# Performance work log

Hardware: AMD Instinct MI355X
Metric: run time of the kernel (lower is better)

Reference implementation:

```python
import jax, jax.numpy as jnp
import numpy as np

CHANNELS = 512
GROUPS = 32
EPS = 1e-5


def setup_inputs() -> dict:
    key = jax.random.key(0)
    ks = jax.random.split(key, 7)
    C = CHANNELS
    x = jax.random.normal(ks[0], (32, C, 32, 32), dtype=jnp.float32)
    norm_w = jax.random.normal(ks[1], (C,), dtype=jnp.float32) * 0.02 + 1.0
    norm_b = jax.random.normal(ks[2], (C,), dtype=jnp.float32) * 0.02
    # 1x1 convs stored as (out_channels, in_channels)
    qkv_w = jax.random.normal(ks[3], (3 * C, C), dtype=jnp.float32) * (C ** -0.5)
    qkv_b = jax.random.normal(ks[4], (3 * C,), dtype=jnp.float32) * 0.02
    proj_w = jax.random.normal(ks[5], (C, C), dtype=jnp.float32) * (C ** -0.5)
    proj_b = jax.random.normal(ks[6], (C,), dtype=jnp.float32) * 0.02
    return {"x": x, "norm_w": norm_w, "norm_b": norm_b,
            "qkv_w": qkv_w, "qkv_b": qkv_b,
            "proj_w": proj_w, "proj_b": proj_b}


def _group_norm(x, w, b):
    B, C, H, W = x.shape
    xg = x.reshape(B, GROUPS, C // GROUPS, H, W)
    mean = xg.mean(axis=(2, 3, 4), keepdims=True)
    var = xg.var(axis=(2, 3, 4), keepdims=True)
    xn = ((xg - mean) * jax.lax.rsqrt(var + EPS)).reshape(B, C, H, W)
    return xn * w[None, :, None, None] + b[None, :, None, None]


def reference(x, norm_w, norm_b, qkv_w, qkv_b, proj_w, proj_b):
    B, C, H, W = x.shape
    scale = C ** (-0.5)
    h = _group_norm(x, norm_w, norm_b)
    # 1x1 conv == per-pixel linear: (B,C,H,W) -> (B,3C,H,W)
    qkv = jnp.einsum('bchw,oc->bohw', h, qkv_w) + qkv_b[None, :, None, None]
    qkv = qkv.reshape(B, 3, C, H * W)
    q, k, v = qkv[:, 0], qkv[:, 1], qkv[:, 2]  # each (B, C, N)
    # attn[b, i, j] = softmax_j( q[:, i] . k[:, j] * scale )
    scores = jnp.einsum('bcn,bcm->bnm', q, k) * scale  # (B, N, N)
    attn = jax.nn.softmax(scores, axis=-1)
    # h[b, c, i] = sum_j v[b, c, j] * attn[b, i, j]
    hout = jnp.einsum('bcm,bnm->bcn', v, attn).reshape(B, C, H, W)
    out = x + jnp.einsum('bchw,oc->bohw', hout, proj_w) + proj_b[None, :, None, None]
    return out
```

## Files before the change

kernel.cpp:

```cpp
#include <hip/hip_runtime.h>
#include <math.h>

#define B_ 32
#define C_ 512
#define G_ 32
#define N_ 1024
#define OC3_ 1536
#define EPS_ 1e-5f

typedef __attribute__((ext_vector_type(8))) short short8;
typedef __attribute__((ext_vector_type(4))) float f32x4;

__device__ inline unsigned short f2bf(float f) {
    unsigned u = __builtin_bit_cast(unsigned, f);
    u += 0x7fffu + ((u >> 16) & 1u);
    return (unsigned short)(u >> 16);
}
__device__ inline unsigned pack2(float lo, float hi) {
    return (unsigned)f2bf(lo) | ((unsigned)f2bf(hi) << 16);
}
__device__ inline float bf2f(unsigned short u) {
    return __builtin_bit_cast(float, ((unsigned)u) << 16);
}

typedef const __attribute__((address_space(1))) unsigned int* gas_u32;
typedef __attribute__((address_space(3))) unsigned int* las_u32;
__device__ __forceinline__ void cp16(unsigned short* lds, const unsigned short* g) {
    __builtin_amdgcn_global_load_lds((gas_u32)g, (las_u32)lds, 16, 0, 0);
}

__device__ __forceinline__ void xcd_decode(int bid, int nbpb, int nbz,
                                           int& bz, int& local) {
    if ((nbz & 7) == 0) {
        int xcd = bid & 7;
        int rest = bid >> 3;
        local = rest % nbpb;
        bz = (rest / nbpb) * 8 + xcd;
    } else {
        bz = bid / nbpb;
        local = bid % nbpb;
    }
}

__global__ __launch_bounds__(256) void prep_kernel(
    const float* __restrict__ x, float* __restrict__ stats,
    const float* __restrict__ qkv_w, unsigned short* __restrict__ wqkv,
    const float* __restrict__ proj_w, unsigned short* __restrict__ wproj)
{
    __shared__ float r1[256], r2[256];
    int bid = blockIdx.x;
    if (bid < 1024) {
        int bg = bid;
        const float4* xv = (const float4*)(x + (size_t)bg * 16 * N_);
        float s = 0.f, ss = 0.f;
        for (int i = threadIdx.x; i < 4096; i += 256) {
            float4 v = xv[i];
            s  += v.x + v.y + v.z + v.w;
            ss += v.x*v.x + v.y*v.y + v.z*v.z + v.w*v.w;
        }
        r1[threadIdx.x] = s; r2[threadIdx.x] = ss;
        __syncthreads();
        for (int off = 128; off > 0; off >>= 1) {
            if (threadIdx.x < off) {
                r1[threadIdx.x] += r1[threadIdx.x + off];
                r2[threadIdx.x] += r2[threadIdx.x + off];
            }
            __syncthreads();
        }
        if (threadIdx.x == 0) {
            float mean = r1[0] * (1.f / 16384.f);
            float var  = r2[0] * (1.f / 16384.f) - mean * mean;
            stats[bg * 2 + 0] = mean;
            stats[bg * 2 + 1] = rsqrtf(var + EPS_);
        }
    } else {
        int i = (bid - 1024) * 256 + threadIdx.x;
        const int nQ = OC3_ * C_ / 4;
        float4 v;
        uint2 o;
        if (i < nQ) {
            v = ((const float4*)qkv_w)[i];
            o.x = pack2(v.x, v.y); o.y = pack2(v.z, v.w);
            ((uint2*)wqkv)[i] = o;
        } else {
            int j = i - nQ;
            v = ((const float4*)proj_w)[j];
            o.x = pack2(v.x, v.y); o.y = pack2(v.z, v.w);
            ((uint2*)wproj)[j] = o;
        }
    }
}

__global__ __launch_bounds__(256) void hhatT_kernel(
    const float* __restrict__ x, const float* __restrict__ stats,
    const float* __restrict__ nw, const float* __restrict__ nbias,
    unsigned short* __restrict__ hhatT, long sH, int b0, int nbz)
{
    int bz, local;
    xcd_decode(blockIdx.x, 128, nbz, bz, local);
    int b = b0 + bz;
    int nt = (local & 15) * 64, ct = (local >> 4) * 64;
    const float* xb = x + (size_t)b * C_ * N_;
    const float* st = stats + b * 2 * G_;

    __shared__ float T[64][65];
    int tid = threadIdx.x;

    #pragma unroll
    for (int p = 0; p < 4; ++p) {
        int c = p * 16 + (tid >> 4);
        int n4 = (tid & 15) * 4;
        float4 v = *(const float4*)&xb[(size_t)(ct + c) * N_ + nt + n4];
        int g = (ct + c) >> 4;
        float w0 = nw[ct + c] * st[g * 2 + 1];
        float bb = nbias[ct + c] - st[g * 2] * w0;
        T[c][n4]   = v.x * w0 + bb;
        T[c][n4+1] = v.y * w0 + bb;
        T[c][n4+2] = v.z * w0 + bb;
        T[c][n4+3] = v.w * w0 + bb;
    }
    __syncthreads();
    #pragma unroll
    for (int p = 0; p < 2; ++p) {
        int n  = p * 32 + (tid >> 3);
        int c8 = (tid & 7) * 8;
        short8 s;
        #pragma unroll
        for (int u = 0; u < 8; ++u) s[u] = (short)f2bf(T[c8 + u][n]);
        *(short8*)&hhatT[(size_t)bz * sH + (size_t)(nt + n) * C_ + ct + c8] = s;
    }
}

template<int EPI>
__global__ __launch_bounds__(256) void gemm128(
    const unsigned short* __restrict__ A, long sA, int lda,
    const unsigned short* __restrict__ B, long sB, int ldb,
    void* __restrict__ Dv, long sD, int ldd,
    const float* __restrict__ bias,
    const float* __restrict__ aux, long sAux,
    int K, float scale, int gx, int gy, int nbz)
{
    int bz, local;
    xcd_decode(blockIdx.x, gx * gy, nbz, bz, local);

    int bx, by;
    bool p2 = false;
    if constexpr (EPI == 5) {
        p2 = local >= 64;
        int li = p2 ? local - 64 : local;
        bx = p2 ? (li & 3) : (li & 7);
        by = p2 ? (li >> 2) : (li >> 3);
    } else {
        bx = local % gx;
        by = local / gx;
    }

    const unsigned short *Ab, *Bb;
    if constexpr (EPI == 5) {
        if (p2) {
            Ab = B + (size_t)(1024 + bx * 128) * ldb;
            Bb = A + (size_t)bz * sA + (size_t)by * 128 * lda;
        } else {
            Ab = A + (size_t)bz * sA + (size_t)bx * 128 * lda;
            Bb = B + (size_t)by * 128 * ldb;
        }
    } else {
        Ab = A + (size_t)bz * sA + (size_t)bx * 128 * lda;
        Bb = B + (size_t)bz * sB + (size_t)by * 128 * ldb;
    }

    __shared__ __align__(16) unsigned short smem[8][4096];

    int tid = threadIdx.x;
    int w = tid >> 6, lane = tid & 63;
    int lm = lane & 15, q = lane >> 4;
    int wrow = (w >> 1) * 64, wcol = (w & 1) * 64;

    f32x4 acc[4][4];
    #pragma unroll
    for (int i = 0; i < 4; ++i)
        #pragma unroll
        for (int j = 0; j < 4; ++j) acc[i][j] = (f32x4)(0.f);

    int srow = tid >> 2;
    int skc  = (((tid & 3) ^ ((tid >> 3) & 3))) * 8;
    int fco  = (q ^ ((lm >> 1) & 3)) * 8;

    const unsigned short* a0p = Ab + (size_t)srow        * lda + skc;
    const unsigned short* a1p = Ab + (size_t)(64 + srow) * lda + skc;
    const unsigned short* b0p = Bb + (size_t)srow        * ldb + skc;
    const unsigned short* b1p = Bb + (size_t)(64 + srow) * ldb + skc;

    {
        cp16(&smem[0][tid * 8],        a0p);
        cp16(&smem[0][2048 + tid * 8], a1p);
        cp16(&smem[1][tid * 8],        a0p + 32);
        cp16(&smem[1][2048 + tid * 8], a1p + 32);
        cp16(&smem[4][tid * 8],        b0p);
        cp16(&smem[4][2048 + tid * 8], b1p);
        cp16(&smem[5][tid * 8],        b0p + 32);
        cp16(&smem[5][2048 + tid * 8], b1p + 32);
    }

    int nIter = K >> 6;
    for (int it = 0; it < nIter; ++it) {
        int cur = it & 1;
        __syncthreads();
        if (it + 1 < nIter) {
            int off = (it + 1) * 64;
            int nxt = cur ^ 1;
            cp16(&smem[nxt * 2][tid * 8],            a0p + off);
            cp16(&smem[nxt * 2][2048 + tid * 8],     a1p + off);
            cp16(&smem[nxt * 2 + 1][tid * 8],        a0p + off + 32);
            cp16(&smem[nxt * 2 + 1][2048 + tid * 8], a1p + off + 32);
            cp16(&smem[4 + nxt * 2][tid * 8],            b0p + off);
            cp16(&smem[4 + nxt * 2][2048 + tid * 8],     b1p + off);
            cp16(&smem[4 + nxt * 2 + 1][tid * 8],        b0p + off + 32);
            cp16(&smem[4 + nxt * 2 + 1][2048 + tid * 8], b1p + off + 32);
        }
        #pragma unroll
        for (int s = 0; s < 2; ++s) {
            const unsigned short* As = smem[cur * 2 + s];
            const unsigned short* Bs = smem[4 + cur * 2 + s];
            short8 af[4], bf[4];
            #pragma unroll
            for (int i = 0; i < 4; ++i)
                af[i] = *(const short8*)&As[(wrow + i * 16 + lm) * 32 + fco];
            #pragma unroll
            for (int j = 0; j < 4; ++j)
                bf[j] = *(const short8*)&Bs[(wcol + j * 16 + lm) * 32 + fco];
            #pragma unroll
            for (int i = 0; i < 4; ++i)
                #pragma unroll
                for (int j = 0; j < 4; ++j)
                    acc[i][j] = __builtin_amdgcn_mfma_f32_16x16x32_bf16(
                        af[i], bf[j], acc[i][j], 0, 0, 0);
        }
    }

    __syncthreads();

    if constexpr (EPI != 4) {
        unsigned short* Ts = &smem[0][0];
        #pragma unroll
        for (int j = 0; j < 4; ++j) {
            int lc = wcol + j * 16 + lm;
            float cb = 0.f;
            if constexpr (EPI == 5) { if (!p2) cb = bias[by * 128 + lc]; }
            #pragma unroll
            for (int i = 0; i < 4; ++i) {
                #pragma unroll
                for (int r = 0; r < 4; ++r) {
                    int lr = wrow + i * 16 + q * 4 + r;
                    float vle = acc[i][j][r];
                    if constexpr (EPI == 2) vle *= scale;
                    else if constexpr (EPI == 5)
                        vle += p2 ? bias[1024 + bx * 128 + lr] : cb;
                    Ts[lr * 128 + (lc ^ (q << 4))] = f2bf(vle);
                }
            }
        }
        __syncthreads();
        size_t doff = 0;
        if constexpr (EPI == 5) { if (p2) doff = (size_t)(1u << 20); }
        unsigned short* Dp = (unsigned short*)Dv + doff +
            (size_t)bz * sD + (size_t)(bx * 128) * ldd + by * 128;
        #pragma unroll
        for (int k = 0; k < 8; ++k) {
            int flat = k * 2048 + tid * 8;
            int rr = flat >> 7, cc = flat & 127;
            short8 vv = *(const short8*)&Ts[flat ^ (w << 4)];
            *(short8*)&Dp[(size_t)rr * ldd + cc] = vv;
        }
    } else {
        float* Ts32 = (float*)&smem[0][0];
        float* Dp = (float*)Dv + (size_t)bz * sD + (size_t)(bx * 128) * ldd + by * 128;
        const float* Ap = aux + (size_t)bz * sAux + (size_t)(bx * 128) * ldd + by * 128;
        #pragma unroll
        for (int h = 0; h < 2; ++h) {
            if (h) __syncthreads();
            if ((w & 1) == h) {
                #pragma unroll
                for (int j = 0; j < 4; ++j) {
                    int lch = j * 16 + lm;
                    #pragma unroll
                    for (int i = 0; i < 4; ++i) {
                        #pragma unroll
                        for (int r = 0; r < 4; ++r) {
                            int lr = wrow + i * 16 + q * 4 + r;
                            int wkey = (lr >> 2) & 7;
                            Ts32[lr * 64 + (lch ^ (wkey << 3))] =
                                acc[i][j][r] + bias[bx * 128 + lr];
                        }
                    }
                }
            }
            __syncthreads();
            #pragma unroll
            for (int k = 0; k < 8; ++k) {
                int flat = k * 1024 + tid * 4;
                int rr = flat >> 6, cc = flat & 63;
                int key = (4 * k + w) & 7;
                f32x4 vv = *(const f32x4*)&Ts32[flat ^ (key << 3)];
                size_t go = (size_t)rr * ldd + h * 64 + cc;
                f32x4 av = *(const f32x4*)&Ap[go];
                *(f32x4*)&Dp[go] = vv + av;
            }
        }
    }
}

__global__ __launch_bounds__(256) void softmax_kernel(
    unsigned short* __restrict__ sc, long sSc, int nbz)
{
    int bz, local;
    xcd_decode(blockIdx.x, 256, nbz, bz, local);
    int row = local * 4 + (threadIdx.x >> 6);
    int lane = threadIdx.x & 63;
    unsigned short* p = sc + (size_t)bz * sSc + (size_t)row * N_ + lane * 16;

    short8 s0 = *(const short8*)p;
    short8 s1 = *(const short8*)(p + 8);
    float v[16];
    #pragma unroll
    for (int i = 0; i < 8; ++i) {
        v[i]     = bf2f((unsigned short)s0[i]);
        v[8 + i] = bf2f((unsigned short)s1[i]);
    }
    float m = v[0];
    #pragma unroll
    for (int i = 1; i < 16; ++i) m = fmaxf(m, v[i]);
    #pragma unroll
    for (int off = 32; off > 0; off >>= 1) m = fmaxf(m, __shfl_xor(m, off, 64));

    float sum = 0.f;
    #pragma unroll
    for (int i = 0; i < 16; ++i) { v[i] = __expf(v[i] - m); sum += v[i]; }
    #pragma unroll
    for (int off = 32; off > 0; off >>= 1) sum += __shfl_xor(sum, off, 64);
    float inv = 1.f / sum;

    short8 o0, o1;
    #pragma unroll
    for (int i = 0; i < 8; ++i) {
        o0[i] = (short)f2bf(v[i] * inv);
        o1[i] = (short)f2bf(v[8 + i] * inv);
    }
    *(short8*)p = o0;
    *(short8*)(p + 8) = o1;
}

extern "C" void kernel_launch(void* const* d_in, const int* in_sizes, int n_in,
                              void* d_out, int out_size, void* d_ws, size_t ws_size,
                              hipStream_t stream) {
    const float* x      = (const float*)d_in[0];
    const float* norm_w = (const float*)d_in[1];
    const float* norm_b = (const float*)d_in[2];
    const float* qkv_w  = (const float*)d_in[3];
    const float* qkv_b  = (const float*)d_in[4];
    const float* proj_w = (const float*)d_in[5];
    const float* proj_b = (const float*)d_in[6];
    float* out = (float*)d_out;

    char* ws = (char*)d_ws;
    float* stats = (float*)ws;
    unsigned short* wqkv  = (unsigned short*)(ws + 8192);
    unsigned short* wproj = wqkv + (size_t)OC3_ * C_;
    char* base = (char*)(wproj + (size_t)C_ * C_);
    const size_t fixed = 8192 + (size_t)OC3_ * C_ * 2 + (size_t)C_ * C_ * 2;

    const size_t REG = 6u << 20;
    const long RSH = (long)(REG / 2);

    size_t avail = ws_size > fixed ? ws_size - fixed : 0;
    int chunk = (int)(avail / REG);
    if (chunk < 1) chunk = 1;
    if (chunk > B_) chunk = B_;

    prep_kernel<<<dim3(2048), dim3(256), 0, stream>>>(
        x, stats, qkv_w, wqkv, proj_w, wproj);

    const float scale = 0.044194173824159216f;

    unsigned short* qkT   = (unsigned short*)base;
    unsigned short* vbuf  = (unsigned short*)(base + (2u << 20));
    unsigned short* hhatT = (unsigned short*)(base + (3u << 20));
    unsigned short* houtT = (unsigned short*)(base + (3u << 20));
    unsigned short* sc    = (unsigned short*)(base + (4u << 20));

    for (int b0 = 0; b0 < B_; b0 += chunk) {
        int nb = B_ - b0 < chunk ? B_ - b0 : chunk;

        hhatT_kernel<<<dim3(128 * nb), dim3(256), 0, stream>>>(
            x, stats, norm_w, norm_b, hhatT, RSH, b0, nb);

        gemm128<5><<<dim3(96 * nb), dim3(256), 0, stream>>>(
            hhatT, RSH, C_,  wqkv, 0, C_,
            qkT, RSH, 1024,  qkv_b, nullptr, 0, C_, 0.f, 96, 1, nb);

        gemm128<2><<<dim3(8 * 8 * nb), dim3(256), 0, stream>>>(
            qkT, RSH, 1024,  qkT + 512, RSH, 1024,
            sc, RSH, N_,  nullptr, nullptr, 0, C_, scale, 8, 8, nb);

        softmax_kernel<<<dim3(256 * nb), dim3(256), 0, stream>>>(sc, RSH, nb);

        gemm128<3><<<dim3(8 * 4 * nb), dim3(256), 0, stream>>>(
            sc, RSH, N_,  vbuf, RSH, N_,
            houtT, RSH, C_,  nullptr, nullptr, 0, N_, 0.f, 8, 4, nb);

        gemm128<4><<<dim3(4 * 8 * nb), dim3(256), 0, stream>>>(
            wproj, 0, C_,  houtT, RSH, C_,
            out + (size_t)b0 * C_ * N_, (long)C_ * N_, N_,
            proj_b, x + (size_t)b0 * C_ * N_, (long)C_ * N_, C_, 0.f, 4, 8, nb);
    }
}
```

Baseline: 373.4 us.

## Add 8-wave split-K GEMM for attention scores and PV, batch softmax rows

Adds a 512-thread GEMM kernel that splits K between two 4-wave groups. It uses a 3-stage cp.async pipeline, setprio around the MFMAs, and a shared-memory reduction of the two partial accumulators before the bf16 epilogue. The QK^T and attn·V GEMMs move to this kernel, which is meant to improve latency hiding and occupancy for these small per-batch GEMMs. Softmax now processes 4 rows per wave with a quarter of the blocks, reducing launch and scheduling overhead. The cost is extra LDS traffic for the split-K reduction and larger shared memory use per block.

After: 412.7 us. +10.5%, slower.

```diff
diff --git a/kernel.cpp b/kernel.cpp
--- a/kernel.cpp
+++ b/kernel.cpp
@@ -132,6 +132,135 @@
 }
 
 template<int EPI>
+__global__ __launch_bounds__(512) void gemm8w(
+    const unsigned short* __restrict__ A, long sA, int lda,
+    const unsigned short* __restrict__ B, long sB, int ldb,
+    unsigned short* __restrict__ D, long sD, int ldd,
+    int K, float scale, int gx, int gy, int nbz)
+{
+    int bz, local;
+    xcd_decode(blockIdx.x, gx * gy, nbz, bz, local);
+    int bx = local % gx, by = local / gx;
+
+    const unsigned short* Ab = A + (size_t)bz * sA + (size_t)bx * 128 * lda;
+    const unsigned short* Bb = B + (size_t)bz * sB + (size_t)by * 128 * ldb;
+
+    __shared__ __align__(16) unsigned short smem[49152];
+
+    int tid = threadIdx.x;
+    int w = tid >> 6, lane = tid & 63;
+    int lm = lane & 15, q = lane >> 4;
+    int g = w >> 2;
+    int qd = w & 3;
+    int wrow = (qd >> 1) * 64, wcol = (qd & 1) * 64;
+
+    int H = K >> 6;
+
+    f32x4 acc[4][4];
+    #pragma unroll
+    for (int i = 0; i < 4; ++i)
+        #pragma unroll
+        for (int j = 0; j < 4; ++j) acc[i][j] = (f32x4)(0.f);
+
+    int srow = tid >> 2;
+    int skc  = (((tid & 3) ^ ((srow >> 1) & 3))) * 8;
+    int fco  = (q ^ ((lm >> 1) & 3)) * 8;
+    int td8  = tid * 8;
+
+    const unsigned short* aP0 = Ab + (size_t)srow * lda + skc;
+    const unsigned short* bP0 = Bb + (size_t)srow * ldb + skc;
+    const unsigned short* aP1 = aP0 + H * 32;
+    const unsigned short* bP1 = bP0 + H * 32;
+
+    #define AT_(gg, jj) (smem + ((gg) * 3 + (jj)) * 4096)
+    #define BT_(gg, jj) (smem + 24576 + ((gg) * 3 + (jj)) * 4096)
+
+    cp16(AT_(0,0) + td8, aP0);      cp16(BT_(0,0) + td8, bP0);
+    cp16(AT_(1,0) + td8, aP1);      cp16(BT_(1,0) + td8, bP1);
+    cp16(AT_(0,1) + td8, aP0 + 32); cp16(BT_(0,1) + td8, bP0 + 32);
+    cp16(AT_(1,1) + td8, aP1 + 32); cp16(BT_(1,1) + td8, bP1 + 32);
+    asm volatile("s_waitcnt vmcnt(4)" ::: "memory");
+    __builtin_amdgcn_s_barrier();
+    __builtin_amdgcn_sched_barrier(0);
+
+    int jc = 0;
+    int j2 = 2;
+    for (int i = 0; i < H; ++i) {
+        if (i + 2 < H) {
+            int off = (i + 2) * 32;
+            cp16(AT_(0, j2) + td8, aP0 + off);
+            cp16(BT_(0, j2) + td8, bP0 + off);
+            cp16(AT_(1, j2) + td8, aP1 + off);
+            cp16(BT_(1, j2) + td8, bP1 + off);
+        }
+        const unsigned short* At = AT_(g, jc);
+        const unsigned short* Bt = BT_(g, jc);
+        short8 af[4], bf[4];
+        #pragma unroll
+        for (int ii = 0; ii < 4; ++ii)
+            af[ii] = *(const short8*)&At[(wrow + ii * 16 + lm) * 32 + fco];
+        #pragma unroll
+        for (int jj = 0; jj < 4; ++jj)
+            bf[jj] = *(const short8*)&Bt[(wcol + jj * 16 + lm) * 32 + fco];
+        __builtin_amdgcn_s_setprio(1);
+        #pragma unroll
+        for (int ii = 0; ii < 4; ++ii)
+            #pragma unroll
+            for (int jj = 0; jj < 4; ++jj)
+                acc[ii][jj] = __builtin_amdgcn_mfma_f32_16x16x32_bf16(
+                    af[ii], bf[jj], acc[ii][jj], 0, 0, 0);
+        __builtin_amdgcn_s_setprio(0);
+        if (i + 2 < H) asm volatile("s_waitcnt vmcnt(4)" ::: "memory");
+        else           asm volatile("s_waitcnt vmcnt(0)" ::: "memory");
+        __builtin_amdgcn_s_barrier();
+        __builtin_amdgcn_sched_barrier(0);
+        jc = (jc == 2) ? 0 : jc + 1;
+        j2 = (j2 == 2) ? 0 : j2 + 1;
+    }
+
+    float* Ms = (float*)(smem + 16384) + qd * 4096;
+    if (g == 1) {
+        #pragma unroll
+        for (int ii = 0; ii < 4; ++ii)
+            #pragma unroll
+            for (int jj = 0; jj < 4; ++jj)
+                #pragma unroll
+                for (int r = 0; r < 4; ++r)
+                    Ms[(ii * 16 + q * 4 + r) * 64 + jj * 16 + lm] = acc[ii][jj][r];
+    }
+    __builtin_amdgcn_s_barrier();
+    if (g == 0) {
+        unsigned short* Ts = smem;
+        #pragma unroll
+        for (int jj = 0; jj < 4; ++jj) {
+            int lc = wcol + jj * 16 + lm;
+            #pragma unroll
+            for (int ii = 0; ii < 4; ++ii) {
+                #pragma unroll
+                for (int r = 0; r < 4; ++r) {
+                    int lr = wrow + ii * 16 + q * 4 + r;
+                    float v = acc[ii][jj][r] +
+                              Ms[(ii * 16 + q * 4 + r) * 64 + jj * 16 + lm];
+                    if constexpr (EPI == 2) v *= scale;
+                    Ts[lr * 128 + (lc ^ (q << 4))] = f2bf(v);
+                }
+            }
+        }
+    }
+    __builtin_amdgcn_s_barrier();
+    unsigned short* Dp = D + (size_t)bz * sD + (size_t)(bx * 128) * ldd + by * 128;
+    #pragma unroll
+    for (int k = 0; k < 4; ++k) {
+        int flat = k * 4096 + tid * 8;
+        int rr = flat >> 7, cc = flat & 127;
+        short8 vv = *(const short8*)&smem[flat ^ ((w & 3) << 4)];
+        *(short8*)&Dp[(size_t)rr * ldd + cc] = vv;
+    }
+    #undef AT_
+    #undef BT_
+}
+
+template<int EPI>
 __global__ __launch_bounds__(256) void gemm128(
     const unsigned short* __restrict__ A, long sA, int lda,
     const unsigned short* __restrict__ B, long sB, int ldb,
@@ -191,16 +320,14 @@
     const unsigned short* b0p = Bb + (size_t)srow        * ldb + skc;
     const unsigned short* b1p = Bb + (size_t)(64 + srow) * ldb + skc;
 
-    {
-        cp16(&smem[0][tid * 8],        a0p);
-        cp16(&smem[0][2048 + tid * 8], a1p);
-        cp16(&smem[1][tid * 8],        a0p + 32);
-        cp16(&smem[1][2048 + tid * 8], a1p + 32);
-        cp16(&smem[4][tid * 8],        b0p);
-        cp16(&smem[4][2048 + tid * 8], b1p);
-        cp16(&smem[5][tid * 8],        b0p + 32);
-        cp16(&smem[5][2048 + tid * 8], b1p + 32);
-    }
+    cp16(&smem[0][tid * 8],        a0p);
+    cp16(&smem[0][2048 + tid * 8], a1p);
+    cp16(&smem[1][tid * 8],        a0p + 32);
+    cp16(&smem[1][2048 + tid * 8], a1p + 32);
+    cp16(&smem[4][tid * 8],        b0p);
+    cp16(&smem[4][2048 + tid * 8], b1p);
+    cp16(&smem[5][tid * 8],        b0p + 32);
+    cp16(&smem[5][2048 + tid * 8], b1p + 32);
 
     int nIter = K >> 6;
     for (int it = 0; it < nIter; ++it) {
@@ -253,8 +380,7 @@
                 for (int r = 0; r < 4; ++r) {
                     int lr = wrow + i * 16 + q * 4 + r;
                     float vle = acc[i][j][r];
-                    if constexpr (EPI == 2) vle *= scale;
-                    else if constexpr (EPI == 5)
+                    if constexpr (EPI == 5)
                         vle += p2 ? bias[1024 + bx * 128 + lr] : cb;
                     Ts[lr * 128 + (lc ^ (q << 4))] = f2bf(vle);
                 }
@@ -314,40 +440,43 @@
     unsigned short* __restrict__ sc, long sSc, int nbz)
 {
     int bz, local;
-    xcd_decode(blockIdx.x, 256, nbz, bz, local);
-    int row = local * 4 + (threadIdx.x >> 6);
+    xcd_decode(blockIdx.x, 64, nbz, bz, local);
+    int wid = threadIdx.x >> 6;
     int lane = threadIdx.x & 63;
-    unsigned short* p = sc + (size_t)bz * sSc + (size_t)row * N_ + lane * 16;
-
-    short8 s0 = *(const short8*)p;
-    short8 s1 = *(const short8*)(p + 8);
-    float v[16];
-    #pragma unroll
-    for (int i = 0; i < 8; ++i) {
-        v[i]     = bf2f((unsigned short)s0[i]);
-        v[8 + i] = bf2f((unsigned short)s1[i]);
-    }
-    float m = v[0];
-    #pragma unroll
-    for (int i = 1; i < 16; ++i) m = fmaxf(m, v[i]);
-    #pragma unroll
-    for (int off = 32; off > 0; off >>= 1) m = fmaxf(m, __shfl_xor(m, off, 64));
-
-    float sum = 0.f;
-    #pragma unroll
-    for (int i = 0; i < 16; ++i) { v[i] = __expf(v[i] - m); sum += v[i]; }
-    #pragma unroll
-    for (int off = 32; off > 0; off >>= 1) sum += __shfl_xor(sum, off, 64);
-    float inv = 1.f / sum;
-
-    short8 o0, o1;
-    #pragma unroll
-    for (int i = 0; i < 8; ++i) {
-        o0[i] = (short)f2bf(v[i] * inv);
-        o1[i] = (short)f2bf(v[8 + i] * inv);
-    }
-    *(short8*)p = o0;
-    *(short8*)(p + 8) = o1;
+    int row0 = local * 16 + wid * 4;
+
+    for (int rr = 0; rr < 4; ++rr) {
+        unsigned short* p = sc + (size_t)bz * sSc + (size_t)(row0 + rr) * N_ + lane * 16;
+        short8 s0 = *(const short8*)p;
+        short8 s1 = *(const short8*)(p + 8);
+        float v[16];
+        #pragma unroll
+        for (int i = 0; i < 8; ++i) {
+            v[i]     = bf2f((unsigned short)s0[i]);
+            v[8 + i] = bf2f((unsigned short)s1[i]);
+        }
+        float m = v[0];
+        #pragma unroll
+        for (int i = 1; i < 16; ++i) m = fmaxf(m, v[i]);
+        #pragma unroll
+        for (int off = 32; off > 0; off >>= 1) m = fmaxf(m, __shfl_xor(m, off, 64));
+
+        float sum = 0.f;
+        #pragma unroll
+        for (int i = 0; i < 16; ++i) { v[i] = __expf(v[i] - m); sum += v[i]; }
+        #pragma unroll
+        for (int off = 32; off > 0; off >>= 1) sum += __shfl_xor(sum, off, 64);
+        float inv = 1.f / sum;
+
+        short8 o0, o1;
+        #pragma unroll
+        for (int i = 0; i < 8; ++i) {
+            o0[i] = (short)f2bf(v[i] * inv);
+            o1[i] = (short)f2bf(v[8 + i] * inv);
+        }
+        *(short8*)p = o0;
+        *(short8*)(p + 8) = o1;
+    }
 }
 
 extern "C" void kernel_launch(void* const* d_in, const int* in_sizes, int n_in,
@@ -398,15 +527,15 @@
             hhatT, RSH, C_,  wqkv, 0, C_,
             qkT, RSH, 1024,  qkv_b, nullptr, 0, C_, 0.f, 96, 1, nb);
 
-        gemm128<2><<<dim3(8 * 8 * nb), dim3(256), 0, stream>>>(
+        gemm8w<2><<<dim3(8 * 8 * nb), dim3(512), 0, stream>>>(
             qkT, RSH, 1024,  qkT + 512, RSH, 1024,
-            sc, RSH, N_,  nullptr, nullptr, 0, C_, scale, 8, 8, nb);
-
-        softmax_kernel<<<dim3(256 * nb), dim3(256), 0, stream>>>(sc, RSH, nb);
-
-        gemm128<3><<<dim3(8 * 4 * nb), dim3(256), 0, stream>>>(
+            sc, RSH, N_,  C_, scale, 8, 8, nb);
+
+        softmax_kernel<<<dim3(64 * nb), dim3(256), 0, stream>>>(sc, RSH, nb);
+
+        gemm8w<3><<<dim3(8 * 4 * nb), dim3(512), 0, stream>>>(
             sc, RSH, N_,  vbuf, RSH, N_,
-            houtT, RSH, C_,  nullptr, nullptr, 0, N_, 0.f, 8, 4, nb);
+            houtT, RSH, C_,  N_, 0.f, 8, 4, nb);
 
         gemm128<4><<<dim3(4 * 8 * nb), dim3(256), 0, stream>>>(
             wproj, 0, C_,  houtT, RSH, C_,
```
